# Kernel optimization log

Measured on AMD Instinct MI355X. Metric: run time of the kernel, lower is better.

## Reference

```python
import jax, jax.numpy as jnp
import numpy as np

N_NODES = 100000
N_EDGES = 1000000
N_INPUT = 64
N_HIDDEN = 64
K = 8


def setup_inputs() -> dict:
    key = jax.random.key(0)
    k1, k2, k3, k4 = jax.random.split(key, 4)
    x = jax.random.normal(k1, (N_NODES, N_INPUT), dtype=jnp.float32)
    edge_index = jax.random.randint(k2, (2, N_EDGES), 0, N_NODES, dtype=jnp.int64)
    # ChebConv has K independent [in, out] weight matrices (Glorot-ish scale) and a bias.
    weight = jax.random.normal(k3, (K, N_INPUT, N_HIDDEN), dtype=jnp.float32) * (1.0 / np.sqrt(N_INPUT))
    bias = jax.random.normal(k4, (N_HIDDEN,), dtype=jnp.float32) * 0.01
    return {"x": x, "edge_index": edge_index, "weight": weight, "bias": bias}


def _cheb_edge_norm(edge_index, num_nodes):
    # PyG ChebConv sym normalization with default lambda_max=2.0:
    #   L_hat = (2/lambda_max) * (I - D^-1/2 A D^-1/2) - I = -D^-1/2 A D^-1/2
    # (the diagonal +1 from the Laplacian and the -1 self-loop cancel exactly).
    src, dst = edge_index[0], edge_index[1]
    ones = jnp.ones(src.shape[0], dtype=jnp.float32)
    deg = jax.ops.segment_sum(ones, src, num_segments=num_nodes)
    deg_inv_sqrt = jnp.where(deg > 0, jax.lax.rsqrt(jnp.maximum(deg, 1.0)), 0.0)
    return -deg_inv_sqrt[src] * deg_inv_sqrt[dst]  # [E]


def reference(x, edge_index, weight, bias):
    num_nodes = x.shape[0]
    src, dst = edge_index[0], edge_index[1]
    norm = _cheb_edge_norm(edge_index, num_nodes)

    def prop(h):  # h: [N, F] -> L_hat @ h via gather-multiply-scatter over edges
        return jax.ops.segment_sum(norm[:, None] * h[src], dst, num_segments=num_nodes)

    # Chebyshev recursion: T0 = x, T1 = L_hat x, Tk = 2 L_hat T_{k-1} - T_{k-2}
    Tx0 = x
    out = Tx0 @ weight[0]
    Tx1 = prop(Tx0)
    out = out + Tx1 @ weight[1]
    for k in range(2, weight.shape[0]):
        Tx2 = 2.0 * prop(Tx1) - Tx0
        out = out + Tx2 @ weight[k]
        Tx0, Tx1 = Tx1, Tx2
    out = out + bias
    # bn=False path: ReLU then dropout (identity in eval mode)
    return jax.nn.relu(out)
```

## Files before the change

kernel.cpp:

```cpp
#include <hip/hip_runtime.h>
#include <hip/hip_bf16.h>

typedef __attribute__((ext_vector_type(8))) short s16x8;
typedef __attribute__((ext_vector_type(4))) float f32x4;

#define HC 48
#define RBH 12800
#define RBS 6400

static __device__ __forceinline__ unsigned short f2bf(float f) {
    unsigned int u = __float_as_uint(f);
    unsigned int r = (u + 0x7FFFu + ((u >> 16) & 1u)) >> 16;
    return (unsigned short)r;
}

__global__ __launch_bounds__(256) void k_hist(const int* __restrict__ eidx,
                                              unsigned short* __restrict__ partials,
                                              int N, int E, int HR) {
    __shared__ unsigned int h[RBH / 2];
    int b = blockIdx.x;
    int job = b / (HR * HC);
    int rc = b % (HR * HC);
    int r = rc / HC, c = rc % HC;
    int lo = r * RBH;
    int nb = min(RBH, N - lo);
    if (nb <= 0) return;
    int nw = (nb + 1) >> 1;
    for (int i = threadIdx.x; i < nw; i += 256) h[i] = 0;
    __syncthreads();
    const int* vals = eidx + (size_t)job * E;
    int e0 = (int)(((long long)E * c / HC) & ~3LL);
    int e1 = (c == HC - 1) ? E : (int)(((long long)E * (c + 1) / HC) & ~3LL);
    int e = e0 + threadIdx.x * 4;
    for (; e + 4 <= e1; e += 1024) {
        int4 v = *reinterpret_cast<const int4*>(vals + e);
        unsigned r0 = (unsigned)(v.x - lo), r1 = (unsigned)(v.y - lo);
        unsigned r2 = (unsigned)(v.z - lo), r3 = (unsigned)(v.w - lo);
        if (r0 < (unsigned)nb) atomicAdd(&h[r0 >> 1], 1u << ((r0 & 1) << 4));
        if (r1 < (unsigned)nb) atomicAdd(&h[r1 >> 1], 1u << ((r1 & 1) << 4));
        if (r2 < (unsigned)nb) atomicAdd(&h[r2 >> 1], 1u << ((r2 & 1) << 4));
        if (r3 < (unsigned)nb) atomicAdd(&h[r3 >> 1], 1u << ((r3 & 1) << 4));
    }
    if (threadIdx.x == 0)
        for (int t = e1 & ~3; t < e1; ++t) {
            unsigned rel = (unsigned)(vals[t] - lo);
            if (rel < (unsigned)nb) atomicAdd(&h[rel >> 1], 1u << ((rel & 1) << 4));
        }
    __syncthreads();
    unsigned short* outp = partials + ((size_t)(job * HC + c)) * N + lo;
    for (int i = threadIdx.x; i < nb; i += 256)
        outp[i] = (unsigned short)((h[i >> 1] >> ((i & 1) << 4)) & 0xffffu);
}

__global__ __launch_bounds__(1024) void k_rs(const unsigned short* __restrict__ partials,
                                             float* __restrict__ dis,
                                             float* __restrict__ dsi,
                                             int* __restrict__ cnt,
                                             int* __restrict__ incl,
                                             int* __restrict__ bsum, int N) {
    __shared__ int sm[1024];
    int t = threadIdx.x;
    int i = blockIdx.x * 1024 + t;
    int csum = 0;
    if (i < N) {
        int dsum = 0;
        for (int c = 0; c < HC; ++c) {
            dsum += partials[(size_t)c * N + i];
            csum += partials[(size_t)(HC + c) * N + i];
        }
        dis[i] = dsum > 0 ? rsqrtf((float)dsum) : 0.f;
        dsi[i] = dsum > 0 ? sqrtf((float)dsum) : 0.f;
        cnt[i] = csum;
    }
    sm[t] = (i < N) ? csum : 0;
    __syncthreads();
    for (int off = 1; off < 1024; off <<= 1) {
        int add = (t >= off) ? sm[t - off] : 0;
        __syncthreads();
        sm[t] += add;
        __syncthreads();
    }
    if (i < N) incl[i] = sm[t];
    if (t == 1023) bsum[blockIdx.x] = sm[1023];
}

__global__ __launch_bounds__(1024) void k_scan3(const int* __restrict__ cnt,
                                                const int* __restrict__ bsum,
                                                int* __restrict__ rowptr,
                                                const unsigned short* __restrict__ pdst,
                                                int* __restrict__ cbase, int N, int nb) {
    __shared__ int sb[128];
    int t = threadIdx.x;
    if (t < 128) sb[t] = (t < nb) ? bsum[t] : 0;
    __syncthreads();
    for (int off = 1; off < 128; off <<= 1) {
        int add = (t < 128 && t >= off) ? sb[t - off] : 0;
        __syncthreads();
        if (t < 128) sb[t] += add;
        __syncthreads();
    }
    int b = blockIdx.x;
    int boff = (b == 0) ? 0 : sb[b - 1];
    int total = sb[nb - 1];
    int i = b * 1024 + t;
    if (i >= N) return;
    int ex = rowptr[i] - cnt[i] + boff;
    rowptr[i] = ex;
    if (i == N - 1) rowptr[N] = total;
    int run = ex;
    for (int c = 0; c < HC; ++c) {
        size_t idx = (size_t)c * N + i;
        cbase[idx] = run;
        run += pdst[idx];
    }
}

__global__ __launch_bounds__(256) void k_scpk(
        const int* __restrict__ src, const int* __restrict__ dst,
        const int* __restrict__ cbase, int* __restrict__ srcs, int N, int E, int SB,
        const float* __restrict__ x, const float* __restrict__ dis,
        const float* __restrict__ W,
        unsigned short* __restrict__ ysb, unsigned short* __restrict__ wt,
        float* __restrict__ walt, int K, int PSE) {
    __shared__ int cur[RBS];
    if ((int)blockIdx.x < SB) {
        int r = blockIdx.x / HC, c = blockIdx.x % HC;
        int lo = r * RBS;
        int nb = min(RBS, N - lo);
        if (nb <= 0) return;
        for (int i = threadIdx.x; i < nb; i += 256)
            cur[i] = cbase[(size_t)c * N + lo + i];
        __syncthreads();
        int e0 = (int)(((long long)E * c / HC) & ~3LL);
        int e1 = (c == HC - 1) ? E : (int)(((long long)E * (c + 1) / HC) & ~3LL);
        int e = e0 + threadIdx.x * 4;
        for (; e + 4 <= e1; e += 1024) {
            int4 d4 = *reinterpret_cast<const int4*>(dst + e);
            unsigned r0 = (unsigned)(d4.x - lo), r1 = (unsigned)(d4.y - lo);
            unsigned r2 = (unsigned)(d4.z - lo), r3 = (unsigned)(d4.w - lo);
            if (r0 < (unsigned)nb) srcs[atomicAdd(&cur[r0], 1)] = src[e];
            if (r1 < (unsigned)nb) srcs[atomicAdd(&cur[r1], 1)] = src[e + 1];
            if (r2 < (unsigned)nb) srcs[atomicAdd(&cur[r2], 1)] = src[e + 2];
            if (r3 < (unsigned)nb) srcs[atomicAdd(&cur[r3], 1)] = src[e + 3];
        }
        if (threadIdx.x == 0)
            for (int t = e1 & ~3; t < e1; ++t) {
                unsigned rel = (unsigned)(dst[t] - lo);
                if (rel < (unsigned)nb) srcs[atomicAdd(&cur[rel], 1)] = src[t];
            }
    } else {
        int t = (blockIdx.x - SB) * 256 + threadIdx.x;
        int nys = (N + 1) * 32;
        if (t < nys) {
            int row = t >> 5, p = t & 31;
            if (row == N) {
                for (int k = 0; k < K; ++k)
                    *(unsigned*)(ysb + (size_t)k * PSE + ((size_t)N << 6) + (p << 1)) = 0;
                return;
            }
            size_t o = ((size_t)row << 6) + (p << 1);
            float2 v = *reinterpret_cast<const float2*>(x + o);
            float dv = dis[row];
            *(unsigned*)(ysb + o) = (unsigned)f2bf(v.x * dv) | ((unsigned)f2bf(v.y * dv) << 16);
        } else {
            int u = t - nys;
            if (u < K * 4096) {
                float v = W[u];
                int k = u >> 12;
                int r = u & 4095;
                int i = r >> 6;
                int j = r & 63;
                wt[(size_t)j * (K * 64) + (k << 6) + i] = f2bf(v);
            } else if (u < K * 4096 + 4096) {
                int u2 = u - K * 4096;
                float s = 0.f;
                for (int k = 0; k < K; k += 2)
                    s += ((k & 3) == 0 ? 1.f : -1.f) * W[k * 4096 + u2];
                walt[u2] = s;
            }
        }
    }
}

static __device__ __forceinline__ void addrow(float* acc, uint4 t) {
    acc[0] += __uint_as_float(t.x << 16);
    acc[1] += __uint_as_float(t.x & 0xffff0000u);
    acc[2] += __uint_as_float(t.y << 16);
    acc[3] += __uint_as_float(t.y & 0xffff0000u);
    acc[4] += __uint_as_float(t.z << 16);
    acc[5] += __uint_as_float(t.z & 0xffff0000u);
    acc[6] += __uint_as_float(t.w << 16);
    acc[7] += __uint_as_float(t.w & 0xffff0000u);
}

__global__ __launch_bounds__(256) void k_prop(
        const unsigned short* __restrict__ Ysin,
        const unsigned short* __restrict__ Ysm2,
        unsigned short* __restrict__ Ysout,
        const int* __restrict__ rowptr, const int* __restrict__ srcs,
        const float* __restrict__ dis,
        int N, int E, float scale, float beta) {
    int gt = blockIdx.x * blockDim.x + threadIdx.x;
    int wave0 = (gt >> 6) << 3;
    int lane = gt & 63;
    int g = lane >> 3;
    int i = lane & 7;
    int node = wave0 + g;
    bool live = node < N;
    int rs = 0, deg = 0;
    if (live) {
        rs = rowptr[node];
        deg = rowptr[node + 1] - rs;
    }
    int wmax = deg;
#pragma unroll
    for (int m = 8; m <= 32; m <<= 1) {
        int o = __shfl_xor(wmax, m);
        wmax = o > wmax ? o : wmax;
    }
    float acc[8];
#pragma unroll
    for (int j = 0; j < 8; ++j) acc[j] = 0.f;
    for (int e = 0; e < wmax; e += 8) {
        int b = rs + e;
        int s[8];
#pragma unroll
        for (int q = 0; q < 8; ++q)
            s[q] = (e + q < deg) ? srcs[min(b + q, E - 1)] : N;
        uint4 t[8];
#pragma unroll
        for (int q = 0; q < 8; ++q)
            t[q] = *reinterpret_cast<const uint4*>(Ysin + ((size_t)s[q] << 6) + (i << 3));
#pragma unroll
        for (int q = 0; q < 8; ++q) addrow(acc, t[q]);
    }
    if (live) {
        float dv = dis[node];
        float sc = -scale * dv * dv;
        size_t base = ((size_t)node << 6) + (i << 3);
        float r[8];
#pragma unroll
        for (int j = 0; j < 8; ++j) r[j] = sc * acc[j];
        if (beta != 0.f) {
            uint4 pv = *reinterpret_cast<const uint4*>(Ysm2 + base);
            r[0] = fmaf(beta, __uint_as_float(pv.x << 16), r[0]);
            r[1] = fmaf(beta, __uint_as_float(pv.x & 0xffff0000u), r[1]);
            r[2] = fmaf(beta, __uint_as_float(pv.y << 16), r[2]);
            r[3] = fmaf(beta, __uint_as_float(pv.y & 0xffff0000u), r[3]);
            r[4] = fmaf(beta, __uint_as_float(pv.z << 16), r[4]);
            r[5] = fmaf(beta, __uint_as_float(pv.z & 0xffff0000u), r[5]);
            r[6] = fmaf(beta, __uint_as_float(pv.w << 16), r[6]);
            r[7] = fmaf(beta, __uint_as_float(pv.w & 0xffff0000u), r[7]);
        }
        uint4 ov;
        ov.x = (unsigned)f2bf(r[0]) | ((unsigned)f2bf(r[1]) << 16);
        ov.y = (unsigned)f2bf(r[2]) | ((unsigned)f2bf(r[3]) << 16);
        ov.z = (unsigned)f2bf(r[4]) | ((unsigned)f2bf(r[5]) << 16);
        ov.w = (unsigned)f2bf(r[6]) | ((unsigned)f2bf(r[7]) << 16);
        *reinterpret_cast<uint4*>(Ysout + base) = ov;
    }
}

template <int KS>
__global__ __launch_bounds__(256) void k_gemm(const unsigned short* __restrict__ tb,
                                              const unsigned short* __restrict__ wt,
                                              const float* __restrict__ bias,
                                              const float* __restrict__ dsi,
                                              const float* __restrict__ x,
                                              const float* __restrict__ walt,
                                              float* __restrict__ out,
                                              int N, int PSE) {
    constexpr int NB = KS / 2;
    __shared__ unsigned short lds_b[KS * 512];
    __shared__ unsigned short lds_a[KS * 256 * 8];
    int tid = threadIdx.x;
    int lane = tid & 63;
    int w = tid >> 6;
    int l16 = lane & 15;
    int quad = lane >> 4;
    const int KI = KS * 32;

    {
        const unsigned short* wrow = wt + (size_t)(w * 16 + l16) * KI + quad * 8;
#pragma unroll
        for (int ks = 0; ks < KS; ++ks) {
            s16x8 v = *reinterpret_cast<const s16x8*>(wrow + ks * 32);
            *reinterpret_cast<s16x8*>(lds_a + (ks * 256 + tid) * 8) = v;
        }
    }
    f32x4 bias4 = *reinterpret_cast<const f32x4*>(bias + w * 16 + quad * 4);

    int ntiles = N >> 4;
    for (int t = blockIdx.x; t < ntiles; t += gridDim.x) {
        const char* tilebase = (const char*)tb + (size_t)t * 2048;
#pragma unroll
        for (int inst = 0; inst < 2 * NB; ++inst) {
            if ((inst & 3) != w) continue;
            int kbuf = inst >> 1;
            int j = inst & 1;
            int p = j * 64 + lane;
            int nrow = p >> 3;
            int s = (p & 7) ^ (nrow & 7);
            const char* g = tilebase + (size_t)kbuf * PSE * 2 + nrow * 128 + s * 16;
            __builtin_amdgcn_global_load_lds(
                (const __attribute__((address_space(1))) unsigned int*)g,
                (__attribute__((address_space(3))) unsigned int*)(lds_b + inst * 512),
                16, 0, 0);
        }
        __syncthreads();
        f32x4 acc = {0.f, 0.f, 0.f, 0.f};
#pragma unroll
        for (int ks = 0; ks < KS; ++ks) {
            s16x8 af = *reinterpret_cast<const s16x8*>(lds_a + (ks * 256 + tid) * 8);
            int kbuf = ks >> 1, half = ks & 1;
            int sph = (half * 4 + quad) ^ (l16 & 7);
            s16x8 bf = *reinterpret_cast<const s16x8*>(
                lds_b + kbuf * 1024 + l16 * 64 + sph * 8);
            acc = __builtin_amdgcn_mfma_f32_16x16x32_bf16(af, bf, acc, 0, 0, 0);
        }
        int row = t * 16 + l16;
        float dvi = dsi[row];
        float* orow = out + (size_t)row * 64 + w * 16 + quad * 4;
        f32x4 r;
        if (dvi != 0.f) {
#pragma unroll
            for (int q = 0; q < 4; ++q) {
                float v = fmaf(acc[q], dvi, bias4[q]);
                r[q] = v > 0.f ? v : 0.f;
            }
        } else {
            const float* xr = x + (size_t)row * 64;
            float rr[4] = {bias4[0], bias4[1], bias4[2], bias4[3]};
            for (int j = 0; j < 64; ++j) {
                float xv = xr[j];
                const float* wr = walt + j * 64 + w * 16 + quad * 4;
#pragma unroll
                for (int q = 0; q < 4; ++q) rr[q] = fmaf(xv, wr[q], rr[q]);
            }
#pragma unroll
            for (int q = 0; q < 4; ++q) r[q] = rr[q] > 0.f ? rr[q] : 0.f;
        }
        *reinterpret_cast<f32x4*>(orow) = r;
        __syncthreads();
    }
}

extern "C" void kernel_launch(void* const* d_in, const int* in_sizes, int n_in,
                              void* d_out, int out_size, void* d_ws, size_t ws_size,
                              hipStream_t stream) {
    const float* x    = (const float*)d_in[0];
    const int*   eidx = (const int*)d_in[1];
    const float* W    = (const float*)d_in[2];
    const float* bias = (const float*)d_in[3];
    float* out = (float*)d_out;

    const int NF = in_sizes[0];
    const int N  = NF / 64;
    const int E  = in_sizes[1] / 2;
    const int K  = in_sizes[2] / 4096;

    const int* src = eidx;
    const int* dst = eidx + E;

    const int PSE = (N + 1) * 64;

    char* ws = (char*)d_ws;
    size_t off = 0;
    auto alloc = [&](size_t bytes) -> char* {
        char* p = ws + off;
        off = (off + bytes + 255) & ~(size_t)255;
        return p;
    };
    unsigned short* Ysb = (unsigned short*)alloc((size_t)K * PSE * 2);
    unsigned short* Wt = (unsigned short*)alloc((size_t)64 * K * 64 * 2);
    float* Walt  = (float*)alloc(4096 * 4);
    int*   srcs   = (int*)alloc((size_t)E * 4);
    int*   rowptr = (int*)alloc((size_t)(N + 1) * 4);
    int*   cnt    = (int*)alloc((size_t)N * 4);
    unsigned short* partials = (unsigned short*)alloc((size_t)2 * HC * N * 2);
    int*   cbase  = (int*)alloc((size_t)HC * N * 4);
    float* dis  = (float*)alloc((size_t)N * 4);
    float* dsi  = (float*)alloc((size_t)N * 4);
    int*   bsum = (int*)alloc(1024);
    (void)ws_size; (void)n_in; (void)out_size;

    int HR = (N + RBH - 1) / RBH;
    int SR = (N + RBS - 1) / RBS;
    const unsigned short* pdst = partials + (size_t)HC * N;

    k_hist<<<2 * HR * HC, 256, 0, stream>>>(eidx, partials, N, E, HR);
    int nb = (N + 1023) / 1024;
    k_rs<<<nb, 1024, 0, stream>>>(partials, dis, dsi, cnt, rowptr, bsum, N);
    k_scan3<<<nb, 1024, 0, stream>>>(cnt, bsum, rowptr, pdst, cbase, N, nb);

    int SB = SR * HC;
    int packn = (N + 1) * 32 + K * 4096 + 4096;
    int pblk = (packn + 255) / 256;
    k_scpk<<<SB + pblk, 256, 0, stream>>>(src, dst, cbase, srcs, N, E, SB,
                                          x, dis, W, Ysb, Wt, Walt, K, PSE);

    int waves = (N + 7) / 8;
    int pblocks = (waves * 64 + 255) / 256;
    for (int p = 1; p < K; ++p) {
        float scale = (p == 1) ? 1.f : 2.f;
        float beta  = (p == 1) ? 0.f : -1.f;
        const unsigned short* Ysin = Ysb + (size_t)(p - 1) * PSE;
        const unsigned short* Ysm2 = Ysb + (size_t)(p >= 2 ? p - 2 : 0) * PSE;
        k_prop<<<pblocks, 256, 0, stream>>>(
            Ysin, Ysm2, Ysb + (size_t)p * PSE,
            rowptr, srcs, dis, N, E, scale, beta);
    }

    if (K == 8)      k_gemm<16><<<512, 256, 0, stream>>>(Ysb, Wt, bias, dsi, x, Walt, out, N, PSE);
    else if (K == 4) k_gemm<8><<<512, 256, 0, stream>>>(Ysb, Wt, bias, dsi, x, Walt, out, N, PSE);
    else if (K == 2) k_gemm<4><<<512, 256, 0, stream>>>(Ysb, Wt, bias, dsi, x, Walt, out, N, PSE);
    else if (K == 1) k_gemm<2><<<512, 256, 0, stream>>>(Ysb, Wt, bias, dsi, x, Walt, out, N, PSE);
}
```

Baseline: 317.4 us.

## Sort nodes by in-degree so each propagation wave handles similar-degree rows

Builds a counting-sort permutation of nodes by in-degree (capped at 63): a histogram is accumulated in k_rs, prefix offsets are computed in k_scan3, and a new k_perm kernel scatters node ids. k_prop then reads node indices through this permutation, so the 8 nodes sharing a wave have similar degree and less loop divergence from the per-wave max-degree loop. The cost is an extra kernel launch, a memset, global atomics, and scattered output writes and rowptr reads, since neighbouring lanes no longer handle contiguous nodes.

```diff
diff --git a/kernel.cpp b/kernel.cpp
--- a/kernel.cpp
+++ b/kernel.cpp
@@ -57,10 +57,13 @@
                                              float* __restrict__ dsi,
                                              int* __restrict__ cnt,
                                              int* __restrict__ incl,
-                                             int* __restrict__ bsum, int N) {
+                                             int* __restrict__ bsum,
+                                             int* __restrict__ gdh, int N) {
     __shared__ int sm[1024];
+    __shared__ int dh[64];
     int t = threadIdx.x;
     int i = blockIdx.x * 1024 + t;
+    if (t < 64) dh[t] = 0;
     int csum = 0;
     if (i < N) {
         int dsum = 0;
@@ -74,6 +77,7 @@
     }
     sm[t] = (i < N) ? csum : 0;
     __syncthreads();
+    if (i < N) atomicAdd(&dh[min(csum, 63)], 1);
     for (int off = 1; off < 1024; off <<= 1) {
         int add = (t >= off) ? sm[t - off] : 0;
         __syncthreads();
@@ -82,13 +86,16 @@
     }
     if (i < N) incl[i] = sm[t];
     if (t == 1023) bsum[blockIdx.x] = sm[1023];
+    if (t < 64 && dh[t] > 0) atomicAdd(&gdh[t], dh[t]);
 }
 
 __global__ __launch_bounds__(1024) void k_scan3(const int* __restrict__ cnt,
                                                 const int* __restrict__ bsum,
                                                 int* __restrict__ rowptr,
                                                 const unsigned short* __restrict__ pdst,
-                                                int* __restrict__ cbase, int N, int nb) {
+                                                int* __restrict__ cbase,
+                                                const int* __restrict__ gdh,
+                                                int* __restrict__ gcur, int N, int nb) {
     __shared__ int sb[128];
     int t = threadIdx.x;
     if (t < 128) sb[t] = (t < nb) ? bsum[t] : 0;
@@ -98,6 +105,10 @@
         __syncthreads();
         if (t < 128) sb[t] += add;
         __syncthreads();
+    }
+    if (blockIdx.x == 0 && t == 0) {
+        int run = 0;
+        for (int b2 = 0; b2 < 64; ++b2) { gcur[b2] = run; run += gdh[b2]; }
     }
     int b = blockIdx.x;
     int boff = (b == 0) ? 0 : sb[b - 1];
@@ -112,6 +123,30 @@
         size_t idx = (size_t)c * N + i;
         cbase[idx] = run;
         run += pdst[idx];
+    }
+}
+
+__global__ __launch_bounds__(1024) void k_perm(const int* __restrict__ cnt,
+                                               int* __restrict__ gcur,
+                                               int* __restrict__ perm, int N) {
+    __shared__ int lh[64];
+    __shared__ int lbase[64];
+    __shared__ int lcur[64];
+    int t = threadIdx.x;
+    int i = blockIdx.x * 1024 + t;
+    if (t < 64) { lh[t] = 0; lcur[t] = 0; }
+    __syncthreads();
+    int bin = 0;
+    if (i < N) {
+        bin = min(cnt[i], 63);
+        atomicAdd(&lh[bin], 1);
+    }
+    __syncthreads();
+    if (t < 64 && lh[t] > 0) lbase[t] = atomicAdd(&gcur[t], lh[t]);
+    __syncthreads();
+    if (i < N) {
+        int r = atomicAdd(&lcur[bin], 1);
+        perm[lbase[bin] + r] = i;
     }
 }
 
@@ -198,17 +233,18 @@
         const unsigned short* __restrict__ Ysm2,
         unsigned short* __restrict__ Ysout,
         const int* __restrict__ rowptr, const int* __restrict__ srcs,
-        const float* __restrict__ dis,
+        const float* __restrict__ dis, const int* __restrict__ perm,
         int N, int E, float scale, float beta) {
     int gt = blockIdx.x * blockDim.x + threadIdx.x;
     int wave0 = (gt >> 6) << 3;
     int lane = gt & 63;
     int g = lane >> 3;
     int i = lane & 7;
-    int node = wave0 + g;
-    bool live = node < N;
-    int rs = 0, deg = 0;
+    int pidx = wave0 + g;
+    bool live = pidx < N;
+    int node = 0, rs = 0, deg = 0;
     if (live) {
+        node = perm[pidx];
         rs = rowptr[node];
         deg = rowptr[node + 1] - rs;
     }
@@ -377,21 +413,26 @@
     int*   srcs   = (int*)alloc((size_t)E * 4);
     int*   rowptr = (int*)alloc((size_t)(N + 1) * 4);
     int*   cnt    = (int*)alloc((size_t)N * 4);
+    int*   perm   = (int*)alloc((size_t)N * 4);
     unsigned short* partials = (unsigned short*)alloc((size_t)2 * HC * N * 2);
     int*   cbase  = (int*)alloc((size_t)HC * N * 4);
     float* dis  = (float*)alloc((size_t)N * 4);
     float* dsi  = (float*)alloc((size_t)N * 4);
     int*   bsum = (int*)alloc(1024);
+    int*   gdh  = (int*)alloc(256);
+    int*   gcur = (int*)alloc(256);
     (void)ws_size; (void)n_in; (void)out_size;
 
     int HR = (N + RBH - 1) / RBH;
     int SR = (N + RBS - 1) / RBS;
     const unsigned short* pdst = partials + (size_t)HC * N;
 
+    hipMemsetAsync(gdh, 0, 256, stream);
     k_hist<<<2 * HR * HC, 256, 0, stream>>>(eidx, partials, N, E, HR);
     int nb = (N + 1023) / 1024;
-    k_rs<<<nb, 1024, 0, stream>>>(partials, dis, dsi, cnt, rowptr, bsum, N);
-    k_scan3<<<nb, 1024, 0, stream>>>(cnt, bsum, rowptr, pdst, cbase, N, nb);
+    k_rs<<<nb, 1024, 0, stream>>>(partials, dis, dsi, cnt, rowptr, bsum, gdh, N);
+    k_scan3<<<nb, 1024, 0, stream>>>(cnt, bsum, rowptr, pdst, cbase, gdh, gcur, N, nb);
+    k_perm<<<nb, 1024, 0, stream>>>(cnt, gcur, perm, N);
 
     int SB = SR * HC;
     int packn = (N + 1) * 32 + K * 4096 + 4096;
@@ -408,7 +449,7 @@
         const unsigned short* Ysm2 = Ysb + (size_t)(p >= 2 ? p - 2 : 0) * PSE;
         k_prop<<<pblocks, 256, 0, stream>>>(
             Ysin, Ysm2, Ysb + (size_t)p * PSE,
-            rowptr, srcs, dis, N, E, scale, beta);
+            rowptr, srcs, dis, perm, N, E, scale, beta);
     }
 
     if (K == 8)      k_gemm<16><<<512, 256, 0, stream>>>(Ysb, Wt, bias, dsi, x, Walt, out, N, PSE);
```

After: 341.7 us. 7.7% more time.
